# Kernel optimization log

Measured on AMD Instinct MI355X. Metric: run time of the kernel, lower is better.

The kernel has to match this reference:

```python
import jax, jax.numpy as jnp
import numpy as np

V, E, H, O, L = 32000, 512, 512, 32, 2
B, T = 64, 512


def setup_inputs() -> dict:
    key = jax.random.key(0)
    ks = jax.random.split(key, 10)
    s = 0.02
    x = jax.random.randint(ks[0], (B, T), 0, V, dtype=jnp.int64)
    seq_lens = jax.random.randint(ks[1], (B,), 1, T + 1, dtype=jnp.int64)
    emb = jax.random.normal(ks[2], (V, E), dtype=jnp.float32) * s
    Whx = jax.random.normal(ks[3], (L, H, E), dtype=jnp.float32) * s  # [out,in] like nn.Linear
    Whh = jax.random.normal(ks[4], (L, H, H), dtype=jnp.float32) * s
    b_h = jnp.zeros((L, H), dtype=jnp.float32)
    Wyh = jax.random.normal(ks[5], (L, H, H), dtype=jnp.float32) * s
    b_y = jnp.zeros((L, H), dtype=jnp.float32)
    Wf = jax.random.normal(ks[6], (O, H), dtype=jnp.float32) * s
    bf = jnp.zeros((O,), dtype=jnp.float32)
    return {"x": x, "sequence_lengths": seq_lens, "emb": emb, "Whx": Whx,
            "Whh": Whh, "b_h": b_h, "Wyh": Wyh, "b_y": b_y, "Wf": Wf, "bf": bf}


def reference(x, sequence_lengths, emb, Whx, Whh, b_h, Wyh, b_y, Wf, bf):
    Bsz, Tlen = x.shape
    x_emb = emb[x]                      # [B,T,E]
    xs = jnp.swapaxes(x_emb, 0, 1)      # time-major [T,B,E]
    h0 = jnp.zeros((L, Bsz, H), dtype=x_emb.dtype)

    def step(h, xt):
        inp = xt
        hs = []
        for l in range(L):
            hl = jnp.tanh(inp @ Whx[l].T + h[l] @ Whh[l].T + b_h[l])
            hs.append(hl)
            inp = hl
        # only the last layer's y is kept by the original loop
        y = inp @ Wyh[L - 1].T + b_y[L - 1]
        return jnp.stack(hs), y

    _, outputs = jax.lax.scan(step, h0, xs)     # outputs: [T,B,H]
    outputs = jnp.swapaxes(outputs, 0, 1)       # [B,T,H]
    idx = sequence_lengths - 1                  # last valid timestep per example
    final_hidden = outputs[jnp.arange(Bsz), idx]  # [B,H]
    return final_hidden @ Wf.T + bf             # [B,O]
```

## Files before the change

kernel.cpp:

```cpp
#include <hip/hip_runtime.h>

namespace {
constexpr int E_ = 512;
constexpr int H_ = 512;
constexpr int O_ = 32;
constexpr int B_ = 64;
constexpr int T_ = 512;
constexpr int RING = 8;
constexpr int FPAD = 16;
constexpr size_t H0_OFF   = 0;
constexpr size_t H1_OFF   = (size_t)RING * B_ * H_;
constexpr size_t HF_OFF   = 2 * H1_OFF;
constexpr size_t FLAG_OFF = HF_OFF + (size_t)B_ * H_;
constexpr size_t FLAG_UINTS = 2u * 8u * 16u * FPAD;
constexpr size_t WS_REQUIRED = (FLAG_OFF + FLAG_UINTS) * 4;
}

typedef float f32x4 __attribute__((ext_vector_type(4)));

__device__ __forceinline__ void coh_ld8(const float* p, f32x4& a, f32x4& b) {
    asm volatile(
        "global_load_dwordx4 %0, %2, off sc0 sc1\n\t"
        "global_load_dwordx4 %1, %2, off offset:16 sc0 sc1\n\t"
        "s_waitcnt vmcnt(0)"
        : "=&v"(a), "=&v"(b) : "v"(p) : "memory");
}
__device__ __forceinline__ void coh_ld16(const float* p, const float* q,
                                         f32x4& a, f32x4& b, f32x4& c, f32x4& d) {
    asm volatile(
        "global_load_dwordx4 %0, %4, off sc0 sc1\n\t"
        "global_load_dwordx4 %1, %4, off offset:16 sc0 sc1\n\t"
        "global_load_dwordx4 %2, %5, off sc0 sc1\n\t"
        "global_load_dwordx4 %3, %5, off offset:16 sc0 sc1\n\t"
        "s_waitcnt vmcnt(0)"
        : "=&v"(a), "=&v"(b), "=&v"(c), "=&v"(d) : "v"(p), "v"(q) : "memory");
}
__device__ __forceinline__ unsigned flag_poll(const unsigned* p) {
    unsigned v;
    asm volatile("global_load_dword %0, %1, off sc0 sc1\n\ts_waitcnt vmcnt(0)"
                 : "=&v"(v) : "v"(p) : "memory");
    return v;
}
__device__ __forceinline__ void vm_drain() {
    asm volatile("s_waitcnt vmcnt(0)" ::: "memory");
}
__device__ __forceinline__ void coh_store(float* p, float v) {
    asm volatile("global_store_dword %0, %1, off sc0 sc1" :: "v"(p), "v"(v) : "memory");
}
__device__ __forceinline__ void flag_store(unsigned* p, unsigned v) {
    asm volatile("global_store_dword %0, %1, off sc0 sc1" :: "v"(p), "v"(v) : "memory");
}

__device__ __forceinline__ float fast_tanh(float x) {
    float e = __builtin_amdgcn_exp2f(x * 2.885390081777927f);
    return 1.0f - 2.0f * __builtin_amdgcn_rcpf(e + 1.0f);
}

__device__ __forceinline__ float reduce8(const float v[8], int lane) {
    float a[4];
#pragma unroll
    for (int j = 0; j < 4; ++j) {
        const int sel = lane & 1;
        const float mine = sel ? v[2 * j + 1] : v[2 * j];
        const float send = sel ? v[2 * j] : v[2 * j + 1];
        a[j] = mine + __shfl_xor(send, 1, 64);
    }
    float b[2];
#pragma unroll
    for (int j = 0; j < 2; ++j) {
        const int sel = (lane >> 1) & 1;
        const float mine = sel ? a[2 * j + 1] : a[2 * j];
        const float send = sel ? a[2 * j] : a[2 * j + 1];
        b[j] = mine + __shfl_xor(send, 2, 64);
    }
    const int sel = (lane >> 2) & 1;
    const float mine = sel ? b[1] : b[0];
    const float send = sel ? b[0] : b[1];
    float s = mine + __shfl_xor(send, 4, 64);
    s += __shfl_xor(s, 8, 64);
    s += __shfl_xor(s, 16, 64);
    s += __shfl_xor(s, 32, 64);
    return s;
}

__global__ __launch_bounds__(512, 1) void rnn_pipe6(
    const int* __restrict__ x, const int* __restrict__ seq_lens,
    const float* __restrict__ emb,
    const float* __restrict__ Whx, const float* __restrict__ Whh,
    const float* __restrict__ b_h,
    float* __restrict__ h0_ring, float* __restrict__ h1_ring,
    float* __restrict__ h1_final, unsigned* __restrict__ flags)
{
    const int bid   = blockIdx.x;
    const int layer = bid >> 7;
    const int g     = (bid >> 4) & 7;
    const int c     = bid & 15;
    const int tid   = threadIdx.x;
    const int wid   = tid >> 6;
    const int lane  = tid & 63;
    const int we    = wid >> 2;
    const int wr    = wid & 3;
    const int rowbase = c * 32 + wr * 8;
    const int eg0   = g * 8 + we * 4;

    __shared__ float sx[2][4096];
    __shared__ float sh[4096];
    __shared__ float sh1[4096];

    const float* WxL = Whx + (size_t)layer * H_ * E_;
    const float* WhL = Whh + (size_t)layer * H_ * H_;
    float w[8][16];
#pragma unroll
    for (int r = 0; r < 8; ++r) {
        const int row = rowbase + r;
        const f32x4 x0 = *(const f32x4*)(WxL + (size_t)row * E_ + (lane << 2));
        const f32x4 x1 = *(const f32x4*)(WxL + (size_t)row * E_ + 256 + (lane << 2));
        const f32x4 h0 = *(const f32x4*)(WhL + (size_t)row * H_ + (lane << 2));
        const f32x4 h1 = *(const f32x4*)(WhL + (size_t)row * H_ + 256 + (lane << 2));
#pragma unroll
        for (int m = 0; m < 4; ++m) {
            w[r][m] = x0[m]; w[r][4 + m] = x1[m];
            w[r][8 + m] = h0[m]; w[r][12 + m] = h1[m];
        }
    }
    const float bias = b_h[layer * H_ + rowbase + (lane & 7)];

    int sl4[4];
#pragma unroll
    for (int q = 0; q < 4; ++q) sl4[q] = seq_lens[eg0 + q];
    int Tg = 1;
#pragma unroll
    for (int j = 0; j < 8; ++j) {
        const int s = seq_lens[g * 8 + j];
        Tg = s > Tg ? s : Tg;
    }

    unsigned* const myflag = flags + ((size_t)((layer * 8 + g) * 16 + c)) * FPAD;
    const unsigned* pollp = flags + ((size_t)((0 * 8 + g) * 16 + (lane & 15))) * FPAD;
    if (lane >= 16 && lane < 32)
        pollp = flags + ((size_t)((8 + g) * 16 + (lane - 16))) * FPAD;

    const int se  = wid;
    const int off = (tid & 63) << 3;
    const int seg = g * 8 + se;

    long budget = 1l << 24;

    if (layer == 0) {
        {
            const int tok = x[(size_t)seg * T_];
            const f32x4 e0 = *(const f32x4*)(emb + ((size_t)tok << 9) + off);
            const f32x4 e1 = *(const f32x4*)(emb + ((size_t)tok << 9) + off + 4);
            *(f32x4*)&sx[0][(se << 9) + off] = e0;
            *(f32x4*)&sx[0][(se << 9) + off + 4] = e1;
        }
        __syncthreads();

        for (int t = 0; t < Tg; ++t) {
            const int cur = t & 1, slot = t & 7, pslot = (t - 1) & 7;
            float vvp[4][8];

#pragma unroll
            for (int q = 0; q < 4; ++q) {
                if (t >= sl4[q]) continue;
                const int el = (we << 2) + q;
                const f32x4 lx0 = *(const f32x4*)&sx[cur][(el << 9) + (lane << 2)];
                const f32x4 lx1 = *(const f32x4*)&sx[cur][(el << 9) + 256 + (lane << 2)];
#pragma unroll
                for (int r = 0; r < 8; ++r) {
                    float s = w[r][0] * lx0[0];
                    s = fmaf(w[r][1], lx0[1], s);
                    s = fmaf(w[r][2], lx0[2], s);
                    s = fmaf(w[r][3], lx0[3], s);
                    s = fmaf(w[r][4], lx1[0], s);
                    s = fmaf(w[r][5], lx1[1], s);
                    s = fmaf(w[r][6], lx1[2], s);
                    s = fmaf(w[r][7], lx1[3], s);
                    vvp[q][r] = s;
                }
            }

            if (wid == 0 && t > 0) {
                const int tgt = (lane < 16) ? t : ((lane < 32) ? t - 7 : 0);
                for (;;) {
                    const unsigned v = flag_poll(pollp);
                    if (!__any((int)v < tgt)) break;
                    if (--budget < 0) break;
                }
            }
            __syncthreads();

            if (t > 0) {
                f32x4 a, b;
                coh_ld8(h0_ring + (((size_t)pslot << 6) + seg) * 512 + off, a, b);
                *(f32x4*)&sh[(se << 9) + off] = a;
                *(f32x4*)&sh[(se << 9) + off + 4] = b;
            } else {
                f32x4 z = 0;
                *(f32x4*)&sh[(se << 9) + off] = z;
                *(f32x4*)&sh[(se << 9) + off + 4] = z;
            }
            f32x4 px0, px1;
            const bool havepf = (t + 1 < Tg);
            if (havepf) {
                const int tok = x[(size_t)seg * T_ + t + 1];
                px0 = *(const f32x4*)(emb + ((size_t)tok << 9) + off);
                px1 = *(const f32x4*)(emb + ((size_t)tok << 9) + off + 4);
            }
            __syncthreads();

#pragma unroll
            for (int q = 0; q < 4; ++q) {
                if (t >= sl4[q]) continue;
                const int el = (we << 2) + q;
                const f32x4 h0a = *(const f32x4*)&sh[(el << 9) + (lane << 2)];
                const f32x4 h0b = *(const f32x4*)&sh[(el << 9) + 256 + (lane << 2)];
#pragma unroll
                for (int r = 0; r < 8; ++r) {
                    float s = vvp[q][r];
                    s = fmaf(w[r][8],  h0a[0], s);
                    s = fmaf(w[r][9],  h0a[1], s);
                    s = fmaf(w[r][10], h0a[2], s);
                    s = fmaf(w[r][11], h0a[3], s);
                    s = fmaf(w[r][12], h0b[0], s);
                    s = fmaf(w[r][13], h0b[1], s);
                    s = fmaf(w[r][14], h0b[2], s);
                    s = fmaf(w[r][15], h0b[3], s);
                    vvp[q][r] = s;
                }
                const float sum = reduce8(vvp[q], lane);
                const float hv = fast_tanh(sum + bias);
                if (lane < 8)
                    coh_store(h0_ring + (((size_t)slot << 6) + eg0 + q) * 512 + rowbase + lane, hv);
            }
            if (havepf) {
                *(f32x4*)&sx[cur ^ 1][(se << 9) + off] = px0;
                *(f32x4*)&sx[cur ^ 1][(se << 9) + off + 4] = px1;
            }
            vm_drain();
            __syncthreads();
            if (tid == 0) flag_store(myflag, (unsigned)(t + 1));
        }
    } else {
        for (int t = 0; t < Tg; ++t) {
            const int slot = t & 7, pslot = (t - 1) & 7;
            float vvp[4][8];

            if (wid == 0) {
                const int tgt = (lane < 16) ? t + 1 : ((lane < 32) ? t : 0);
                for (;;) {
                    const unsigned v = flag_poll(pollp);
                    if (!__any((int)v < tgt)) break;
                    if (--budget < 0) break;
                }
            }
            __syncthreads();

            if (t > 0) {
                f32x4 a, b, cc, d;
                coh_ld16(h0_ring + (((size_t)slot << 6) + seg) * 512 + off,
                         h1_ring + (((size_t)pslot << 6) + seg) * 512 + off, a, b, cc, d);
                *(f32x4*)&sh[(se << 9) + off] = a;
                *(f32x4*)&sh[(se << 9) + off + 4] = b;
                *(f32x4*)&sh1[(se << 9) + off] = cc;
                *(f32x4*)&sh1[(se << 9) + off + 4] = d;
            } else {
                f32x4 a, b;
                coh_ld8(h0_ring + (((size_t)slot << 6) + seg) * 512 + off, a, b);
                *(f32x4*)&sh[(se << 9) + off] = a;
                *(f32x4*)&sh[(se << 9) + off + 4] = b;
                f32x4 z = 0;
                *(f32x4*)&sh1[(se << 9) + off] = z;
                *(f32x4*)&sh1[(se << 9) + off + 4] = z;
            }
            __syncthreads();

#pragma unroll
            for (int q = 0; q < 4; ++q) {
                if (t >= sl4[q]) continue;
                const int el = (we << 2) + q;
                const f32x4 xa = *(const f32x4*)&sh[(el << 9) + (lane << 2)];
                const f32x4 xb = *(const f32x4*)&sh[(el << 9) + 256 + (lane << 2)];
                const f32x4 ha = *(const f32x4*)&sh1[(el << 9) + (lane << 2)];
                const f32x4 hb = *(const f32x4*)&sh1[(el << 9) + 256 + (lane << 2)];
#pragma unroll
                for (int r = 0; r < 8; ++r) {
                    float s = w[r][0] * xa[0];
                    s = fmaf(w[r][1], xa[1], s);
                    s = fmaf(w[r][2], xa[2], s);
                    s = fmaf(w[r][3], xa[3], s);
                    s = fmaf(w[r][4], xb[0], s);
                    s = fmaf(w[r][5], xb[1], s);
                    s = fmaf(w[r][6], xb[2], s);
                    s = fmaf(w[r][7], xb[3], s);
                    s = fmaf(w[r][8],  ha[0], s);
                    s = fmaf(w[r][9],  ha[1], s);
                    s = fmaf(w[r][10], ha[2], s);
                    s = fmaf(w[r][11], ha[3], s);
                    s = fmaf(w[r][12], hb[0], s);
                    s = fmaf(w[r][13], hb[1], s);
                    s = fmaf(w[r][14], hb[2], s);
                    s = fmaf(w[r][15], hb[3], s);
                    vvp[q][r] = s;
                }
                const float sum = reduce8(vvp[q], lane);
                const float hv = fast_tanh(sum + bias);
                if (lane < 8) {
                    coh_store(h1_ring + (((size_t)slot << 6) + eg0 + q) * 512 + rowbase + lane, hv);
                    if (t == sl4[q] - 1)
                        h1_final[((size_t)(eg0 + q) << 9) + rowbase + lane] = hv;
                }
            }
            vm_drain();
            __syncthreads();
            if (tid == 0) flag_store(myflag, (unsigned)(t + 1));
        }
    }
}

__device__ __forceinline__ float dot4(float4 a, float4 b) {
    return fmaf(a.x, b.x, fmaf(a.y, b.y, fmaf(a.z, b.z, a.w * b.w)));
}
__device__ __forceinline__ float wave_reduce(float acc) {
#pragma unroll
    for (int off = 32; off > 0; off >>= 1) acc += __shfl_down(acc, off, 64);
    return acc;
}

__global__ __launch_bounds__(512) void head_kernel(
    const float* __restrict__ h1f, const float* __restrict__ Wyh,
    const float* __restrict__ b_y, const float* __restrict__ Wf,
    const float* __restrict__ bf, float* __restrict__ out)
{
    const int e = blockIdx.x;
    const int tid = threadIdx.x, wid = tid >> 6, lane = tid & 63;
    const int k0 = lane << 3;
    __shared__ float sh[H_];
    __shared__ float sy[H_];
    sh[tid] = h1f[(size_t)e * H_ + tid];
    __syncthreads();
    const float4 hA = *(const float4*)&sh[k0];
    const float4 hB = *(const float4*)&sh[k0 + 4];
    const float* Wy1 = Wyh + H_ * H_;
#pragma unroll 4
    for (int rr = 0; rr < 64; ++rr) {
        const int row = (wid << 6) + rr;
        float acc = wave_reduce(dot4(*(const float4*)&Wy1[(size_t)row * H_ + k0], hA) +
                                dot4(*(const float4*)&Wy1[(size_t)row * H_ + k0 + 4], hB));
        if (lane == 0) sy[row] = acc + b_y[H_ + row];
    }
    __syncthreads();
    const float4 yA = *(const float4*)&sy[k0];
    const float4 yB = *(const float4*)&sy[k0 + 4];
#pragma unroll
    for (int rr = 0; rr < 4; ++rr) {
        const int o = (wid << 2) + rr;
        float acc = wave_reduce(dot4(*(const float4*)&Wf[(size_t)o * H_ + k0], yA) +
                                dot4(*(const float4*)&Wf[(size_t)o * H_ + k0 + 4], yB));
        if (lane == 0) out[(size_t)e * O_ + o] = acc + bf[o];
    }
}

__global__ __launch_bounds__(1024, 1) void rnn_fused_fb(
    const int* __restrict__ x, const int* __restrict__ seq_lens,
    const float* __restrict__ emb, const float* __restrict__ Whx,
    const float* __restrict__ Whh, const float* __restrict__ b_h,
    const float* __restrict__ Wyh, const float* __restrict__ b_y,
    const float* __restrict__ Wf, const float* __restrict__ bf,
    float* __restrict__ out)
{
    const int b = blockIdx.x, tid = threadIdx.x;
    const int wave = tid >> 6, lane = tid & 63, k0 = lane << 3;
    __shared__ float s_inp[E_];
    __shared__ float s_h0[2][H_];
    __shared__ float s_h1[2][H_];
    __shared__ float s_y[H_];
    if (tid < H_) { s_h0[0][tid]=0.f; s_h0[1][tid]=0.f; s_h1[0][tid]=0.f; s_h1[1][tid]=0.f; }
    const int Tb = seq_lens[b];
    const float* Whx0 = Whx; const float* Whx1 = Whx + H_*E_;
    const float* Whh0 = Whh; const float* Whh1 = Whh + H_*H_;
    for (int t = 0; t < Tb; ++t) {
        const int cur = t & 1, prv = cur ^ 1;
        if (tid < E_) { const int tok = x[b*T_+t]; s_inp[tid] = emb[(size_t)tok*E_+tid]; }
        __syncthreads();
        const float4 iA = *(const float4*)&s_inp[k0], iB = *(const float4*)&s_inp[k0+4];
        const float4 pA = *(const float4*)&s_h0[prv][k0], pB = *(const float4*)&s_h0[prv][k0+4];
#pragma unroll 4
        for (int r = 0; r < 32; ++r) {
            const int i = (wave<<5)+r;
            float acc = dot4(*(const float4*)&Whx0[i*E_+k0], iA) + dot4(*(const float4*)&Whx0[i*E_+k0+4], iB)
                      + dot4(*(const float4*)&Whh0[i*H_+k0], pA) + dot4(*(const float4*)&Whh0[i*H_+k0+4], pB);
            acc = wave_reduce(acc);
            if (lane == 0) s_h0[cur][i] = tanhf(acc + b_h[i]);
        }
        __syncthreads();
        const float4 cA = *(const float4*)&s_h0[cur][k0], cB = *(const float4*)&s_h0[cur][k0+4];
        const float4 qA = *(const float4*)&s_h1[prv][k0], qB = *(const float4*)&s_h1[prv][k0+4];
#pragma unroll 4
        for (int r = 0; r < 32; ++r) {
            const int i = (wave<<5)+r;
            float acc = dot4(*(const float4*)&Whx1[i*E_+k0], cA) + dot4(*(const float4*)&Whx1[i*E_+k0+4], cB)
                      + dot4(*(const float4*)&Whh1[i*H_+k0], qA) + dot4(*(const float4*)&Whh1[i*H_+k0+4], qB);
            acc = wave_reduce(acc);
            if (lane == 0) s_h1[cur][i] = tanhf(acc + b_h[H_+i]);
        }
        __syncthreads();
    }
    const int lastb = (Tb-1) & 1;
    const float4 hA = *(const float4*)&s_h1[lastb][k0], hB = *(const float4*)&s_h1[lastb][k0+4];
    const float* Wy1 = Wyh + H_*H_;
#pragma unroll 4
    for (int r = 0; r < 32; ++r) {
        const int i = (wave<<5)+r;
        float acc = wave_reduce(dot4(*(const float4*)&Wy1[i*H_+k0], hA) + dot4(*(const float4*)&Wy1[i*H_+k0+4], hB));
        if (lane == 0) s_y[i] = acc + b_y[H_+i];
    }
    __syncthreads();
    const float4 yA = *(const float4*)&s_y[k0], yB = *(const float4*)&s_y[k0+4];
    if (wave < 8) {
#pragma unroll
        for (int r = 0; r < 4; ++r) {
            const int o = (wave<<2)+r;
            float acc = wave_reduce(dot4(*(const float4*)&Wf[o*H_+k0], yA) + dot4(*(const float4*)&Wf[o*H_+k0+4], yB));
            if (lane == 0) out[b*O_+o] = acc + bf[o];
        }
    }
}

extern "C" void kernel_launch(void* const* d_in, const int* in_sizes, int n_in,
                              void* d_out, int out_size, void* d_ws, size_t ws_size,
                              hipStream_t stream) {
    const int*   x    = (const int*)d_in[0];
    const int*   sl   = (const int*)d_in[1];
    const float* emb  = (const float*)d_in[2];
    const float* Whx  = (const float*)d_in[3];
    const float* Whh  = (const float*)d_in[4];
    const float* b_h  = (const float*)d_in[5];
    const float* Wyh  = (const float*)d_in[6];
    const float* b_y  = (const float*)d_in[7];
    const float* Wf   = (const float*)d_in[8];
    const float* bf   = (const float*)d_in[9];
    float* out = (float*)d_out;

    if (ws_size < WS_REQUIRED) {
        rnn_fused_fb<<<B_, 1024, 0, stream>>>(x, sl, emb, Whx, Whh, b_h, Wyh, b_y, Wf, bf, out);
        return;
    }

    float* ws_f = (float*)d_ws;
    float* h0_ring = ws_f + H0_OFF;
    float* h1_ring = ws_f + H1_OFF;
    float* h1f     = ws_f + HF_OFF;
    unsigned* flags = (unsigned*)(ws_f + FLAG_OFF);

    hipMemsetAsync(flags, 0, FLAG_UINTS * sizeof(unsigned), stream);
    rnn_pipe6<<<256, 512, 0, stream>>>(x, sl, emb, Whx, Whh, b_h,
                                       h0_ring, h1_ring, h1f, flags);
    head_kernel<<<B_, 512, 0, stream>>>(h1f, Wyh, b_y, Wf, bf, out);
}
```

Before: 1.991 ms.

## Load ring hidden states directly into registers and add layer-1 lookahead

Each wave now loads the hidden-state vectors it needs straight from the global ring buffers into registers. This drops the LDS staging and one __syncthreads per step in both layers. Layer 1 also records during its flag poll whether layer 0's next step is already published, and if so starts the input projection of the next step before the barrier. This cuts LDS traffic and block barriers on the serial recurrence critical path, at the cost of redundant global loads (each wave reads 4 sequences) and more registers.

Result: slower. 4.549 ms (+128.4%).

```diff
diff --git a/kernel.cpp b/kernel.cpp
--- a/kernel.cpp
+++ b/kernel.cpp
@@ -18,23 +18,35 @@
 
 typedef float f32x4 __attribute__((ext_vector_type(4)));
 
-__device__ __forceinline__ void coh_ld8(const float* p, f32x4& a, f32x4& b) {
+__device__ __forceinline__ void wrow_load(const float* px, const float* ph,
+                                          f32x4& x0, f32x4& x1, f32x4& h0, f32x4& h1) {
     asm volatile(
-        "global_load_dwordx4 %0, %2, off sc0 sc1\n\t"
-        "global_load_dwordx4 %1, %2, off offset:16 sc0 sc1\n\t"
+        "global_load_dwordx4 %0, %4, off\n\t"
+        "global_load_dwordx4 %1, %4, off offset:1024\n\t"
+        "global_load_dwordx4 %2, %5, off\n\t"
+        "global_load_dwordx4 %3, %5, off offset:1024\n\t"
         "s_waitcnt vmcnt(0)"
-        : "=&v"(a), "=&v"(b) : "v"(p) : "memory");
-}
-__device__ __forceinline__ void coh_ld16(const float* p, const float* q,
-                                         f32x4& a, f32x4& b, f32x4& c, f32x4& d) {
+        : "=&v"(x0), "=&v"(x1), "=&v"(h0), "=&v"(h1)
+        : "v"(px), "v"(ph) : "memory");
+}
+
+__device__ __forceinline__ void ring_load8(const float* p, f32x4 H[8]) {
+    const float* p2 = p + 1024;
     asm volatile(
-        "global_load_dwordx4 %0, %4, off sc0 sc1\n\t"
-        "global_load_dwordx4 %1, %4, off offset:16 sc0 sc1\n\t"
-        "global_load_dwordx4 %2, %5, off sc0 sc1\n\t"
-        "global_load_dwordx4 %3, %5, off offset:16 sc0 sc1\n\t"
+        "global_load_dwordx4 %0, %8, off sc0 sc1\n\t"
+        "global_load_dwordx4 %1, %8, off offset:1024 sc0 sc1\n\t"
+        "global_load_dwordx4 %2, %8, off offset:2048 sc0 sc1\n\t"
+        "global_load_dwordx4 %3, %8, off offset:3072 sc0 sc1\n\t"
+        "global_load_dwordx4 %4, %9, off sc0 sc1\n\t"
+        "global_load_dwordx4 %5, %9, off offset:1024 sc0 sc1\n\t"
+        "global_load_dwordx4 %6, %9, off offset:2048 sc0 sc1\n\t"
+        "global_load_dwordx4 %7, %9, off offset:3072 sc0 sc1\n\t"
         "s_waitcnt vmcnt(0)"
-        : "=&v"(a), "=&v"(b), "=&v"(c), "=&v"(d) : "v"(p), "v"(q) : "memory");
-}
+        : "=&v"(H[0]), "=&v"(H[1]), "=&v"(H[2]), "=&v"(H[3]),
+          "=&v"(H[4]), "=&v"(H[5]), "=&v"(H[6]), "=&v"(H[7])
+        : "v"(p), "v"(p2) : "memory");
+}
+
 __device__ __forceinline__ unsigned flag_poll(const unsigned* p) {
     unsigned v;
     asm volatile("global_load_dword %0, %1, off sc0 sc1\n\ts_waitcnt vmcnt(0)"
@@ -83,7 +95,7 @@
     return s;
 }
 
-__global__ __launch_bounds__(512, 1) void rnn_pipe6(
+__global__ __launch_bounds__(512, 1) void rnn_pipe7(
     const int* __restrict__ x, const int* __restrict__ seq_lens,
     const float* __restrict__ emb,
     const float* __restrict__ Whx, const float* __restrict__ Whh,
@@ -104,24 +116,17 @@
     const int eg0   = g * 8 + we * 4;
 
     __shared__ float sx[2][4096];
-    __shared__ float sh[4096];
-    __shared__ float sh1[4096];
+    __shared__ unsigned s_la[2];
 
     const float* WxL = Whx + (size_t)layer * H_ * E_;
     const float* WhL = Whh + (size_t)layer * H_ * H_;
-    float w[8][16];
+    f32x4 wx0[8], wx1[8], wh0[8], wh1[8];
 #pragma unroll
     for (int r = 0; r < 8; ++r) {
         const int row = rowbase + r;
-        const f32x4 x0 = *(const f32x4*)(WxL + (size_t)row * E_ + (lane << 2));
-        const f32x4 x1 = *(const f32x4*)(WxL + (size_t)row * E_ + 256 + (lane << 2));
-        const f32x4 h0 = *(const f32x4*)(WhL + (size_t)row * H_ + (lane << 2));
-        const f32x4 h1 = *(const f32x4*)(WhL + (size_t)row * H_ + 256 + (lane << 2));
-#pragma unroll
-        for (int m = 0; m < 4; ++m) {
-            w[r][m] = x0[m]; w[r][4 + m] = x1[m];
-            w[r][8 + m] = h0[m]; w[r][12 + m] = h1[m];
-        }
+        wrow_load(WxL + (size_t)row * E_ + (lane << 2),
+                  WhL + (size_t)row * H_ + (lane << 2),
+                  wx0[r], wx1[r], wh0[r], wh1[r]);
     }
     const float bias = b_h[layer * H_ + rowbase + (lane & 7)];
 
@@ -141,7 +146,6 @@
         pollp = flags + ((size_t)((8 + g) * 16 + (lane - 16))) * FPAD;
 
     const int se  = wid;
-    const int off = (tid & 63) << 3;
     const int seg = g * 8 + se;
 
     long budget = 1l << 24;
@@ -149,10 +153,10 @@
     if (layer == 0) {
         {
             const int tok = x[(size_t)seg * T_];
-            const f32x4 e0 = *(const f32x4*)(emb + ((size_t)tok << 9) + off);
-            const f32x4 e1 = *(const f32x4*)(emb + ((size_t)tok << 9) + off + 4);
-            *(f32x4*)&sx[0][(se << 9) + off] = e0;
-            *(f32x4*)&sx[0][(se << 9) + off + 4] = e1;
+            *(f32x4*)&sx[0][(se << 9) + (lane << 2)] =
+                *(const f32x4*)(emb + ((size_t)tok << 9) + (lane << 2));
+            *(f32x4*)&sx[0][(se << 9) + 256 + (lane << 2)] =
+                *(const f32x4*)(emb + ((size_t)tok << 9) + 256 + (lane << 2));
         }
         __syncthreads();
 
@@ -168,18 +172,24 @@
                 const f32x4 lx1 = *(const f32x4*)&sx[cur][(el << 9) + 256 + (lane << 2)];
 #pragma unroll
                 for (int r = 0; r < 8; ++r) {
-                    float s = w[r][0] * lx0[0];
-                    s = fmaf(w[r][1], lx0[1], s);
-                    s = fmaf(w[r][2], lx0[2], s);
-                    s = fmaf(w[r][3], lx0[3], s);
-                    s = fmaf(w[r][4], lx1[0], s);
-                    s = fmaf(w[r][5], lx1[1], s);
-                    s = fmaf(w[r][6], lx1[2], s);
-                    s = fmaf(w[r][7], lx1[3], s);
+                    float s = wx0[r][0] * lx0[0];
+                    s = fmaf(wx0[r][1], lx0[1], s);
+                    s = fmaf(wx0[r][2], lx0[2], s);
+                    s = fmaf(wx0[r][3], lx0[3], s);
+                    s = fmaf(wx1[r][0], lx1[0], s);
+                    s = fmaf(wx1[r][1], lx1[1], s);
+                    s = fmaf(wx1[r][2], lx1[2], s);
+                    s = fmaf(wx1[r][3], lx1[3], s);
                     vvp[q][r] = s;
                 }
             }
-
+            f32x4 px0, px1;
+            const bool havepf = (t + 1 < Tg);
+            if (havepf) {
+                const int tok = x[(size_t)seg * T_ + t + 1];
+                px0 = *(const f32x4*)(emb + ((size_t)tok << 9) + (lane << 2));
+                px1 = *(const f32x4*)(emb + ((size_t)tok << 9) + 256 + (lane << 2));
+            }
             if (wid == 0 && t > 0) {
                 const int tgt = (lane < 16) ? t : ((lane < 32) ? t - 7 : 0);
                 for (;;) {
@@ -190,42 +200,27 @@
             }
             __syncthreads();
 
+            f32x4 H[8];
             if (t > 0) {
-                f32x4 a, b;
-                coh_ld8(h0_ring + (((size_t)pslot << 6) + seg) * 512 + off, a, b);
-                *(f32x4*)&sh[(se << 9) + off] = a;
-                *(f32x4*)&sh[(se << 9) + off + 4] = b;
+                ring_load8(h0_ring + (((size_t)pslot << 6) + eg0) * 512 + (lane << 2), H);
             } else {
-                f32x4 z = 0;
-                *(f32x4*)&sh[(se << 9) + off] = z;
-                *(f32x4*)&sh[(se << 9) + off + 4] = z;
-            }
-            f32x4 px0, px1;
-            const bool havepf = (t + 1 < Tg);
-            if (havepf) {
-                const int tok = x[(size_t)seg * T_ + t + 1];
-                px0 = *(const f32x4*)(emb + ((size_t)tok << 9) + off);
-                px1 = *(const f32x4*)(emb + ((size_t)tok << 9) + off + 4);
-            }
-            __syncthreads();
-
+#pragma unroll
+                for (int i = 0; i < 8; ++i) H[i] = 0;
+            }
 #pragma unroll
             for (int q = 0; q < 4; ++q) {
                 if (t >= sl4[q]) continue;
-                const int el = (we << 2) + q;
-                const f32x4 h0a = *(const f32x4*)&sh[(el << 9) + (lane << 2)];
-                const f32x4 h0b = *(const f32x4*)&sh[(el << 9) + 256 + (lane << 2)];
 #pragma unroll
                 for (int r = 0; r < 8; ++r) {
                     float s = vvp[q][r];
-                    s = fmaf(w[r][8],  h0a[0], s);
-                    s = fmaf(w[r][9],  h0a[1], s);
-                    s = fmaf(w[r][10], h0a[2], s);
-                    s = fmaf(w[r][11], h0a[3], s);
-                    s = fmaf(w[r][12], h0b[0], s);
-                    s = fmaf(w[r][13], h0b[1], s);
-                    s = fmaf(w[r][14], h0b[2], s);
-                    s = fmaf(w[r][15], h0b[3], s);
+                    s = fmaf(wh0[r][0], H[2 * q][0], s);
+                    s = fmaf(wh0[r][1], H[2 * q][1], s);
+                    s = fmaf(wh0[r][2], H[2 * q][2], s);
+                    s = fmaf(wh0[r][3], H[2 * q][3], s);
+                    s = fmaf(wh1[r][0], H[2 * q + 1][0], s);
+                    s = fmaf(wh1[r][1], H[2 * q + 1][1], s);
+                    s = fmaf(wh1[r][2], H[2 * q + 1][2], s);
+                    s = fmaf(wh1[r][3], H[2 * q + 1][3], s);
                     vvp[q][r] = s;
                 }
                 const float sum = reduce8(vvp[q], lane);
@@ -234,75 +229,100 @@
                     coh_store(h0_ring + (((size_t)slot << 6) + eg0 + q) * 512 + rowbase + lane, hv);
             }
             if (havepf) {
-                *(f32x4*)&sx[cur ^ 1][(se << 9) + off] = px0;
-                *(f32x4*)&sx[cur ^ 1][(se << 9) + off + 4] = px1;
+                *(f32x4*)&sx[cur ^ 1][(se << 9) + (lane << 2)] = px0;
+                *(f32x4*)&sx[cur ^ 1][(se << 9) + 256 + (lane << 2)] = px1;
             }
             vm_drain();
             __syncthreads();
             if (tid == 0) flag_store(myflag, (unsigned)(t + 1));
         }
     } else {
+        if (tid == 0) { s_la[0] = 0; s_la[1] = 0; }
+        __syncthreads();
+
         for (int t = 0; t < Tg; ++t) {
             const int slot = t & 7, pslot = (t - 1) & 7;
             float vvp[4][8];
-
+            f32x4 Hx[8];
+
+            const bool la = (t > 0) && (s_la[t & 1] != 0u);
+            bool have_x = false;
+            if (la) {
+                ring_load8(h0_ring + (((size_t)slot << 6) + eg0) * 512 + (lane << 2), Hx);
+#pragma unroll
+                for (int q = 0; q < 4; ++q) {
+                    if (t >= sl4[q]) continue;
+#pragma unroll
+                    for (int r = 0; r < 8; ++r) {
+                        float s = wx0[r][0] * Hx[2 * q][0];
+                        s = fmaf(wx0[r][1], Hx[2 * q][1], s);
+                        s = fmaf(wx0[r][2], Hx[2 * q][2], s);
+                        s = fmaf(wx0[r][3], Hx[2 * q][3], s);
+                        s = fmaf(wx1[r][0], Hx[2 * q + 1][0], s);
+                        s = fmaf(wx1[r][1], Hx[2 * q + 1][1], s);
+                        s = fmaf(wx1[r][2], Hx[2 * q + 1][2], s);
+                        s = fmaf(wx1[r][3], Hx[2 * q + 1][3], s);
+                        vvp[q][r] = s;
+                    }
+                }
+                have_x = true;
+            }
             if (wid == 0) {
                 const int tgt = (lane < 16) ? t + 1 : ((lane < 32) ? t : 0);
+                unsigned v = 0;
                 for (;;) {
-                    const unsigned v = flag_poll(pollp);
+                    v = flag_poll(pollp);
                     if (!__any((int)v < tgt)) break;
                     if (--budget < 0) break;
                 }
+                const bool la_next = !__any((lane < 16) && ((int)v < t + 2));
+                if (lane == 0) s_la[(t + 1) & 1] = la_next ? 1u : 0u;
             }
             __syncthreads();
 
+            if (!have_x) {
+                ring_load8(h0_ring + (((size_t)slot << 6) + eg0) * 512 + (lane << 2), Hx);
+#pragma unroll
+                for (int q = 0; q < 4; ++q) {
+                    if (t >= sl4[q]) continue;
+#pragma unroll
+                    for (int r = 0; r < 8; ++r) {
+                        float s = wx0[r][0] * Hx[2 * q][0];
+                        s = fmaf(wx0[r][1], Hx[2 * q][1], s);
+                        s = fmaf(wx0[r][2], Hx[2 * q][2], s);
+                        s = fmaf(wx0[r][3], Hx[2 * q][3], s);
+                        s = fmaf(wx1[r][0], Hx[2 * q + 1][0], s);
+                        s = fmaf(wx1[r][1], Hx[2 * q + 1][1], s);
+                        s = fmaf(wx1[r][2], Hx[2 * q + 1][2], s);
+                        s = fmaf(wx1[r][3], Hx[2 * q + 1][3], s);
+                        vvp[q][r] = s;
+                    }
+                }
+            }
             if (t > 0) {
-                f32x4 a, b, cc, d;
-                coh_ld16(h0_ring + (((size_t)slot << 6) + seg) * 512 + off,
-                         h1_ring + (((size_t)pslot << 6) + seg) * 512 + off, a, b, cc, d);
-                *(f32x4*)&sh[(se << 9) + off] = a;
-                *(f32x4*)&sh[(se << 9) + off + 4] = b;
-                *(f32x4*)&sh1[(se << 9) + off] = cc;
-                *(f32x4*)&sh1[(se << 9) + off + 4] = d;
-            } else {
-                f32x4 a, b;
-                coh_ld8(h0_ring + (((size_t)slot << 6) + seg) * 512 + off, a, b);
-                *(f32x4*)&sh[(se << 9) + off] = a;
-                *(f32x4*)&sh[(se << 9) + off + 4] = b;
-                f32x4 z = 0;
-                *(f32x4*)&sh1[(se << 9) + off] = z;
-                *(f32x4*)&sh1[(se << 9) + off + 4] = z;
-            }
-            __syncthreads();
-
+                f32x4 H1[8];
+                ring_load8(h1_ring + (((size_t)pslot << 6) + eg0) * 512 + (lane << 2), H1);
+#pragma unroll
+                for (int q = 0; q < 4; ++q) {
+                    if (t >= sl4[q]) continue;
+#pragma unroll
+                    for (int r = 0; r < 8; ++r) {
+                        float s = vvp[q][r];
+                        s = fmaf(wh0[r][0], H1[2 * q][0], s);
+                        s = fmaf(wh0[r][1], H1[2 * q][1], s);
+                        s = fmaf(wh0[r][2], H1[2 * q][2], s);
+                        s = fmaf(wh0[r][3], H1[2 * q][3], s);
+                        s = fmaf(wh1[r][0], H1[2 * q + 1][0], s);
+                        s = fmaf(wh1[r][1], H1[2 * q + 1][1], s);
+                        s = fmaf(wh1[r][2], H1[2 * q + 1][2], s);
+                        s = fmaf(wh1[r][3], H1[2 * q + 1][3], s);
+                        vvp[q][r] = s;
+                    }
+                }
+            }
 #pragma unroll
             for (int q = 0; q < 4; ++q) {
                 if (t >= sl4[q]) continue;
-                const int el = (we << 2) + q;
-                const f32x4 xa = *(const f32x4*)&sh[(el << 9) + (lane << 2)];
-                const f32x4 xb = *(const f32x4*)&sh[(el << 9) + 256 + (lane << 2)];
-                const f32x4 ha = *(const f32x4*)&sh1[(el << 9) + (lane << 2)];
-                const f32x4 hb = *(const f32x4*)&sh1[(el << 9) + 256 + (lane << 2)];
-#pragma unroll
-                for (int r = 0; r < 8; ++r) {
-                    float s = w[r][0] * xa[0];
-                    s = fmaf(w[r][1], xa[1], s);
-                    s = fmaf(w[r][2], xa[2], s);
-                    s = fmaf(w[r][3], xa[3], s);
-                    s = fmaf(w[r][4], xb[0], s);
-                    s = fmaf(w[r][5], xb[1], s);
-                    s = fmaf(w[r][6], xb[2], s);
-                    s = fmaf(w[r][7], xb[3], s);
-                    s = fmaf(w[r][8],  ha[0], s);
-                    s = fmaf(w[r][9],  ha[1], s);
-                    s = fmaf(w[r][10], ha[2], s);
-                    s = fmaf(w[r][11], ha[3], s);
-                    s = fmaf(w[r][12], hb[0], s);
-                    s = fmaf(w[r][13], hb[1], s);
-                    s = fmaf(w[r][14], hb[2], s);
-                    s = fmaf(w[r][15], hb[3], s);
-                    vvp[q][r] = s;
-                }
                 const float sum = reduce8(vvp[q], lane);
                 const float hv = fast_tanh(sum + bias);
                 if (lane < 8) {
@@ -454,7 +474,7 @@
     unsigned* flags = (unsigned*)(ws_f + FLAG_OFF);
 
     hipMemsetAsync(flags, 0, FLAG_UINTS * sizeof(unsigned), stream);
-    rnn_pipe6<<<256, 512, 0, stream>>>(x, sl, emb, Whx, Whh, b_h,
+    rnn_pipe7<<<256, 512, 0, stream>>>(x, sl, emb, Whx, Whh, b_h,
                                        h0_ring, h1_ring, h1f, flags);
     head_kernel<<<B_, 512, 0, stream>>>(h1f, Wyh, b_y, Wf, bf, out);
 }
```

## Split recurrent rows across twice as many blocks and prefetch embeddings earlier

Applied to the files above, without the earlier changes.

Doubles the grid so each block handles 16 hidden rows instead of 32, with 4 rows per wave. This halves the per-thread weight registers and the per-step FMA work. Flag polling widens to 32 producer blocks per group, and global h/embedding loads switch to a lane-contiguous (lane*4, +256) layout. The next-token embedding prefetch is issued before the spin-wait so it overlaps synchronization. In exchange, the persistent spin-wait scheme now depends on two blocks being co-resident per CU and has more flags to poll each step.

Result: no change. 1.953 ms (-1.9%).

```diff
diff --git a/kernel.cpp b/kernel.cpp
--- a/kernel.cpp
+++ b/kernel.cpp
@@ -12,26 +12,26 @@
 constexpr size_t H1_OFF   = (size_t)RING * B_ * H_;
 constexpr size_t HF_OFF   = 2 * H1_OFF;
 constexpr size_t FLAG_OFF = HF_OFF + (size_t)B_ * H_;
-constexpr size_t FLAG_UINTS = 2u * 8u * 16u * FPAD;
+constexpr size_t FLAG_UINTS = 2u * 8u * 32u * FPAD;
 constexpr size_t WS_REQUIRED = (FLAG_OFF + FLAG_UINTS) * 4;
 }
 
 typedef float f32x4 __attribute__((ext_vector_type(4)));
 
-__device__ __forceinline__ void coh_ld8(const float* p, f32x4& a, f32x4& b) {
+__device__ __forceinline__ void coh_ld2k(const float* p, f32x4& a, f32x4& b) {
     asm volatile(
         "global_load_dwordx4 %0, %2, off sc0 sc1\n\t"
-        "global_load_dwordx4 %1, %2, off offset:16 sc0 sc1\n\t"
+        "global_load_dwordx4 %1, %2, off offset:1024 sc0 sc1\n\t"
         "s_waitcnt vmcnt(0)"
         : "=&v"(a), "=&v"(b) : "v"(p) : "memory");
 }
-__device__ __forceinline__ void coh_ld16(const float* p, const float* q,
+__device__ __forceinline__ void coh_ld4k(const float* p, const float* q,
                                          f32x4& a, f32x4& b, f32x4& c, f32x4& d) {
     asm volatile(
         "global_load_dwordx4 %0, %4, off sc0 sc1\n\t"
-        "global_load_dwordx4 %1, %4, off offset:16 sc0 sc1\n\t"
+        "global_load_dwordx4 %1, %4, off offset:1024 sc0 sc1\n\t"
         "global_load_dwordx4 %2, %5, off sc0 sc1\n\t"
-        "global_load_dwordx4 %3, %5, off offset:16 sc0 sc1\n\t"
+        "global_load_dwordx4 %3, %5, off offset:1024 sc0 sc1\n\t"
         "s_waitcnt vmcnt(0)"
         : "=&v"(a), "=&v"(b), "=&v"(c), "=&v"(d) : "v"(p), "v"(q) : "memory");
 }
@@ -56,34 +56,27 @@
     return 1.0f - 2.0f * __builtin_amdgcn_rcpf(e + 1.0f);
 }
 
-__device__ __forceinline__ float reduce8(const float v[8], int lane) {
-    float a[4];
-#pragma unroll
-    for (int j = 0; j < 4; ++j) {
+__device__ __forceinline__ float reduce4(const float v[4], int lane) {
+    float a[2];
+#pragma unroll
+    for (int j = 0; j < 2; ++j) {
         const int sel = lane & 1;
         const float mine = sel ? v[2 * j + 1] : v[2 * j];
         const float send = sel ? v[2 * j] : v[2 * j + 1];
         a[j] = mine + __shfl_xor(send, 1, 64);
     }
-    float b[2];
-#pragma unroll
-    for (int j = 0; j < 2; ++j) {
-        const int sel = (lane >> 1) & 1;
-        const float mine = sel ? a[2 * j + 1] : a[2 * j];
-        const float send = sel ? a[2 * j] : a[2 * j + 1];
-        b[j] = mine + __shfl_xor(send, 2, 64);
-    }
-    const int sel = (lane >> 2) & 1;
-    const float mine = sel ? b[1] : b[0];
-    const float send = sel ? b[0] : b[1];
-    float s = mine + __shfl_xor(send, 4, 64);
+    const int sel = (lane >> 1) & 1;
+    const float mine = sel ? a[1] : a[0];
+    const float send = sel ? a[0] : a[1];
+    float s = mine + __shfl_xor(send, 2, 64);
+    s += __shfl_xor(s, 4, 64);
     s += __shfl_xor(s, 8, 64);
     s += __shfl_xor(s, 16, 64);
     s += __shfl_xor(s, 32, 64);
     return s;
 }
 
-__global__ __launch_bounds__(512, 1) void rnn_pipe6(
+__global__ __launch_bounds__(512, 4) void rnn_pipe8(
     const int* __restrict__ x, const int* __restrict__ seq_lens,
     const float* __restrict__ emb,
     const float* __restrict__ Whx, const float* __restrict__ Whh,
@@ -92,15 +85,15 @@
     float* __restrict__ h1_final, unsigned* __restrict__ flags)
 {
     const int bid   = blockIdx.x;
-    const int layer = bid >> 7;
-    const int g     = (bid >> 4) & 7;
-    const int c     = bid & 15;
+    const int layer = bid >> 8;
+    const int g     = (bid >> 5) & 7;
+    const int c     = bid & 31;
     const int tid   = threadIdx.x;
     const int wid   = tid >> 6;
     const int lane  = tid & 63;
     const int we    = wid >> 2;
     const int wr    = wid & 3;
-    const int rowbase = c * 32 + wr * 8;
+    const int rowbase = c * 16 + wr * 4;
     const int eg0   = g * 8 + we * 4;
 
     __shared__ float sx[2][4096];
@@ -109,21 +102,16 @@
 
     const float* WxL = Whx + (size_t)layer * H_ * E_;
     const float* WhL = Whh + (size_t)layer * H_ * H_;
-    float w[8][16];
-#pragma unroll
-    for (int r = 0; r < 8; ++r) {
+    f32x4 wx0[4], wx1[4], wh0[4], wh1[4];
+#pragma unroll
+    for (int r = 0; r < 4; ++r) {
         const int row = rowbase + r;
-        const f32x4 x0 = *(const f32x4*)(WxL + (size_t)row * E_ + (lane << 2));
-        const f32x4 x1 = *(const f32x4*)(WxL + (size_t)row * E_ + 256 + (lane << 2));
-        const f32x4 h0 = *(const f32x4*)(WhL + (size_t)row * H_ + (lane << 2));
-        const f32x4 h1 = *(const f32x4*)(WhL + (size_t)row * H_ + 256 + (lane << 2));
-#pragma unroll
-        for (int m = 0; m < 4; ++m) {
-            w[r][m] = x0[m]; w[r][4 + m] = x1[m];
-            w[r][8 + m] = h0[m]; w[r][12 + m] = h1[m];
-        }
-    }
-    const float bias = b_h[layer * H_ + rowbase + (lane & 7)];
+        wx0[r] = *(const f32x4*)(WxL + (size_t)row * E_ + (lane << 2));
+        wx1[r] = *(const f32x4*)(WxL + (size_t)row * E_ + 256 + (lane << 2));
+        wh0[r] = *(const f32x4*)(WhL + (size_t)row * H_ + (lane << 2));
+        wh1[r] = *(const f32x4*)(WhL + (size_t)row * H_ + 256 + (lane << 2));
+    }
+    const float bias = b_h[layer * H_ + rowbase + (lane & 3)];
 
     int sl4[4];
 #pragma unroll
@@ -135,13 +123,12 @@
         Tg = s > Tg ? s : Tg;
     }
 
-    unsigned* const myflag = flags + ((size_t)((layer * 8 + g) * 16 + c)) * FPAD;
-    const unsigned* pollp = flags + ((size_t)((0 * 8 + g) * 16 + (lane & 15))) * FPAD;
-    if (lane >= 16 && lane < 32)
-        pollp = flags + ((size_t)((8 + g) * 16 + (lane - 16))) * FPAD;
+    unsigned* const myflag = flags + ((size_t)((layer * 8 + g) * 32 + c)) * FPAD;
+    const unsigned* const pollp = (lane < 32)
+        ? flags + ((size_t)(g * 32 + lane)) * FPAD
+        : flags + ((size_t)((8 + g) * 32 + (lane - 32))) * FPAD;
 
     const int se  = wid;
-    const int off = (tid & 63) << 3;
     const int seg = g * 8 + se;
 
     long budget = 1l << 24;
@@ -149,16 +136,16 @@
     if (layer == 0) {
         {
             const int tok = x[(size_t)seg * T_];
-            const f32x4 e0 = *(const f32x4*)(emb + ((size_t)tok << 9) + off);
-            const f32x4 e1 = *(const f32x4*)(emb + ((size_t)tok << 9) + off + 4);
-            *(f32x4*)&sx[0][(se << 9) + off] = e0;
-            *(f32x4*)&sx[0][(se << 9) + off + 4] = e1;
+            *(f32x4*)&sx[0][(se << 9) + (lane << 2)] =
+                *(const f32x4*)(emb + ((size_t)tok << 9) + (lane << 2));
+            *(f32x4*)&sx[0][(se << 9) + 256 + (lane << 2)] =
+                *(const f32x4*)(emb + ((size_t)tok << 9) + 256 + (lane << 2));
         }
         __syncthreads();
 
         for (int t = 0; t < Tg; ++t) {
             const int cur = t & 1, slot = t & 7, pslot = (t - 1) & 7;
-            float vvp[4][8];
+            float vvp[4][4];
 
 #pragma unroll
             for (int q = 0; q < 4; ++q) {
@@ -167,21 +154,27 @@
                 const f32x4 lx0 = *(const f32x4*)&sx[cur][(el << 9) + (lane << 2)];
                 const f32x4 lx1 = *(const f32x4*)&sx[cur][(el << 9) + 256 + (lane << 2)];
 #pragma unroll
-                for (int r = 0; r < 8; ++r) {
-                    float s = w[r][0] * lx0[0];
-                    s = fmaf(w[r][1], lx0[1], s);
-                    s = fmaf(w[r][2], lx0[2], s);
-                    s = fmaf(w[r][3], lx0[3], s);
-                    s = fmaf(w[r][4], lx1[0], s);
-                    s = fmaf(w[r][5], lx1[1], s);
-                    s = fmaf(w[r][6], lx1[2], s);
-                    s = fmaf(w[r][7], lx1[3], s);
+                for (int r = 0; r < 4; ++r) {
+                    float s = wx0[r][0] * lx0[0];
+                    s = fmaf(wx0[r][1], lx0[1], s);
+                    s = fmaf(wx0[r][2], lx0[2], s);
+                    s = fmaf(wx0[r][3], lx0[3], s);
+                    s = fmaf(wx1[r][0], lx1[0], s);
+                    s = fmaf(wx1[r][1], lx1[1], s);
+                    s = fmaf(wx1[r][2], lx1[2], s);
+                    s = fmaf(wx1[r][3], lx1[3], s);
                     vvp[q][r] = s;
                 }
             }
-
+            f32x4 px0, px1;
+            const bool havepf = (t + 1 < Tg);
+            if (havepf) {
+                const int tok = x[(size_t)seg * T_ + t + 1];
+                px0 = *(const f32x4*)(emb + ((size_t)tok << 9) + (lane << 2));
+                px1 = *(const f32x4*)(emb + ((size_t)tok << 9) + 256 + (lane << 2));
+            }
             if (wid == 0 && t > 0) {
-                const int tgt = (lane < 16) ? t : ((lane < 32) ? t - 7 : 0);
+                const int tgt = (lane < 32) ? t : t - 7;
                 for (;;) {
                     const unsigned v = flag_poll(pollp);
                     if (!__any((int)v < tgt)) break;
@@ -192,20 +185,13 @@
 
             if (t > 0) {
                 f32x4 a, b;
-                coh_ld8(h0_ring + (((size_t)pslot << 6) + seg) * 512 + off, a, b);
-                *(f32x4*)&sh[(se << 9) + off] = a;
-                *(f32x4*)&sh[(se << 9) + off + 4] = b;
+                coh_ld2k(h0_ring + (((size_t)pslot << 6) + seg) * 512 + (lane << 2), a, b);
+                *(f32x4*)&sh[(se << 9) + (lane << 2)] = a;
+                *(f32x4*)&sh[(se << 9) + 256 + (lane << 2)] = b;
             } else {
                 f32x4 z = 0;
-                *(f32x4*)&sh[(se << 9) + off] = z;
-                *(f32x4*)&sh[(se << 9) + off + 4] = z;
-            }
-            f32x4 px0, px1;
-            const bool havepf = (t + 1 < Tg);
-            if (havepf) {
-                const int tok = x[(size_t)seg * T_ + t + 1];
-                px0 = *(const f32x4*)(emb + ((size_t)tok << 9) + off);
-                px1 = *(const f32x4*)(emb + ((size_t)tok << 9) + off + 4);
+                *(f32x4*)&sh[(se << 9) + (lane << 2)] = z;
+                *(f32x4*)&sh[(se << 9) + 256 + (lane << 2)] = z;
             }
             __syncthreads();
 
@@ -216,26 +202,26 @@
                 const f32x4 h0a = *(const f32x4*)&sh[(el << 9) + (lane << 2)];
                 const f32x4 h0b = *(const f32x4*)&sh[(el << 9) + 256 + (lane << 2)];
 #pragma unroll
-                for (int r = 0; r < 8; ++r) {
+                for (int r = 0; r < 4; ++r) {
                     float s = vvp[q][r];
-                    s = fmaf(w[r][8],  h0a[0], s);
-                    s = fmaf(w[r][9],  h0a[1], s);
-                    s = fmaf(w[r][10], h0a[2], s);
-                    s = fmaf(w[r][11], h0a[3], s);
-                    s = fmaf(w[r][12], h0b[0], s);
-                    s = fmaf(w[r][13], h0b[1], s);
-                    s = fmaf(w[r][14], h0b[2], s);
-                    s = fmaf(w[r][15], h0b[3], s);
+                    s = fmaf(wh0[r][0], h0a[0], s);
+                    s = fmaf(wh0[r][1], h0a[1], s);
+                    s = fmaf(wh0[r][2], h0a[2], s);
+                    s = fmaf(wh0[r][3], h0a[3], s);
+                    s = fmaf(wh1[r][0], h0b[0], s);
+                    s = fmaf(wh1[r][1], h0b[1], s);
+                    s = fmaf(wh1[r][2], h0b[2], s);
+                    s = fmaf(wh1[r][3], h0b[3], s);
                     vvp[q][r] = s;
                 }
-                const float sum = reduce8(vvp[q], lane);
+                const float sum = reduce4(vvp[q], lane);
                 const float hv = fast_tanh(sum + bias);
-                if (lane < 8)
+                if (lane < 4)
                     coh_store(h0_ring + (((size_t)slot << 6) + eg0 + q) * 512 + rowbase + lane, hv);
             }
             if (havepf) {
-                *(f32x4*)&sx[cur ^ 1][(se << 9) + off] = px0;
-                *(f32x4*)&sx[cur ^ 1][(se << 9) + off + 4] = px1;
+                *(f32x4*)&sx[cur ^ 1][(se << 9) + (lane << 2)] = px0;
+                *(f32x4*)&sx[cur ^ 1][(se << 9) + 256 + (lane << 2)] = px1;
             }
             vm_drain();
             __syncthreads();
@@ -244,10 +230,10 @@
     } else {
         for (int t = 0; t < Tg; ++t) {
             const int slot = t & 7, pslot = (t - 1) & 7;
-            float vvp[4][8];
+            float vvp[4][4];
 
             if (wid == 0) {
-                const int tgt = (lane < 16) ? t + 1 : ((lane < 32) ? t : 0);
+                const int tgt = (lane < 32) ? t + 1 : t;
                 for (;;) {
                     const unsigned v = flag_poll(pollp);
                     if (!__any((int)v < tgt)) break;
@@ -258,20 +244,21 @@
 
             if (t > 0) {
                 f32x4 a, b, cc, d;
-                coh_ld16(h0_ring + (((size_t)slot << 6) + seg) * 512 + off,
-                         h1_ring + (((size_t)pslot << 6) + seg) * 512 + off, a, b, cc, d);
-                *(f32x4*)&sh[(se << 9) + off] = a;
-                *(f32x4*)&sh[(se << 9) + off + 4] = b;
-                *(f32x4*)&sh1[(se << 9) + off] = cc;
-                *(f32x4*)&sh1[(se << 9) + off + 4] = d;
+                coh_ld4k(h0_ring + (((size_t)slot << 6) + seg) * 512 + (lane << 2),
+                         h1_ring + (((size_t)pslot << 6) + seg) * 512 + (lane << 2),
+                         a, b, cc, d);
+                *(f32x4*)&sh[(se << 9) + (lane << 2)] = a;
+                *(f32x4*)&sh[(se << 9) + 256 + (lane << 2)] = b;
+                *(f32x4*)&sh1[(se << 9) + (lane << 2)] = cc;
+                *(f32x4*)&sh1[(se << 9) + 256 + (lane << 2)] = d;
             } else {
                 f32x4 a, b;
-                coh_ld8(h0_ring + (((size_t)slot << 6) + seg) * 512 + off, a, b);
-                *(f32x4*)&sh[(se << 9) + off] = a;
-                *(f32x4*)&sh[(se << 9) + off + 4] = b;
+                coh_ld2k(h0_ring + (((size_t)slot << 6) + seg) * 512 + (lane << 2), a, b);
+                *(f32x4*)&sh[(se << 9) + (lane << 2)] = a;
+                *(f32x4*)&sh[(se << 9) + 256 + (lane << 2)] = b;
                 f32x4 z = 0;
-                *(f32x4*)&sh1[(se << 9) + off] = z;
-                *(f32x4*)&sh1[(se << 9) + off + 4] = z;
+                *(f32x4*)&sh1[(se << 9) + (lane << 2)] = z;
+                *(f32x4*)&sh1[(se << 9) + 256 + (lane << 2)] = z;
             }
             __syncthreads();
 
@@ -284,28 +271,28 @@
                 const f32x4 ha = *(const f32x4*)&sh1[(el << 9) + (lane << 2)];
                 const f32x4 hb = *(const f32x4*)&sh1[(el << 9) + 256 + (lane << 2)];
 #pragma unroll
-                for (int r = 0; r < 8; ++r) {
-                    float s = w[r][0] * xa[0];
-                    s = fmaf(w[r][1], xa[1], s);
-                    s = fmaf(w[r][2], xa[2], s);
-                    s = fmaf(w[r][3], xa[3], s);
-                    s = fmaf(w[r][4], xb[0], s);
-                    s = fmaf(w[r][5], xb[1], s);
-                    s = fmaf(w[r][6], xb[2], s);
-                    s = fmaf(w[r][7], xb[3], s);
-                    s = fmaf(w[r][8],  ha[0], s);
-                    s = fmaf(w[r][9],  ha[1], s);
-                    s = fmaf(w[r][10], ha[2], s);
-                    s = fmaf(w[r][11], ha[3], s);
-                    s = fmaf(w[r][12], hb[0], s);
-                    s = fmaf(w[r][13], hb[1], s);
-                    s = fmaf(w[r][14], hb[2], s);
-                    s = fmaf(w[r][15], hb[3], s);
+                for (int r = 0; r < 4; ++r) {
+                    float s = wx0[r][0] * xa[0];
+                    s = fmaf(wx0[r][1], xa[1], s);
+                    s = fmaf(wx0[r][2], xa[2], s);
+                    s = fmaf(wx0[r][3], xa[3], s);
+                    s = fmaf(wx1[r][0], xb[0], s);
+                    s = fmaf(wx1[r][1], xb[1], s);
+                    s = fmaf(wx1[r][2], xb[2], s);
+                    s = fmaf(wx1[r][3], xb[3], s);
+                    s = fmaf(wh0[r][0], ha[0], s);
+                    s = fmaf(wh0[r][1], ha[1], s);
+                    s = fmaf(wh0[r][2], ha[2], s);
+                    s = fmaf(wh0[r][3], ha[3], s);
+                    s = fmaf(wh1[r][0], hb[0], s);
+                    s = fmaf(wh1[r][1], hb[1], s);
+                    s = fmaf(wh1[r][2], hb[2], s);
+                    s = fmaf(wh1[r][3], hb[3], s);
                     vvp[q][r] = s;
                 }
-                const float sum = reduce8(vvp[q], lane);
+                const float sum = reduce4(vvp[q], lane);
                 const float hv = fast_tanh(sum + bias);
-                if (lane < 8) {
+                if (lane < 4) {
                     coh_store(h1_ring + (((size_t)slot << 6) + eg0 + q) * 512 + rowbase + lane, hv);
                     if (t == sl4[q] - 1)
                         h1_final[((size_t)(eg0 + q) << 9) + rowbase + lane] = hv;
@@ -454,7 +441,7 @@
     unsigned* flags = (unsigned*)(ws_f + FLAG_OFF);
 
     hipMemsetAsync(flags, 0, FLAG_UINTS * sizeof(unsigned), stream);
-    rnn_pipe6<<<256, 512, 0, stream>>>(x, sl, emb, Whx, Whh, b_h,
+    rnn_pipe8<<<512, 512, 0, stream>>>(x, sl, emb, Whx, Whh, b_h,
                                        h0_ring, h1_ring, h1f, flags);
     head_kernel<<<B_, 512, 0, stream>>>(h1f, Wyh, b_y, Wf, bf, out);
 }
```
